# Performance work log

Measured on AMD Instinct MI355X. Metric: run time of the kernel, lower is better.

## Reference

```python
import jax, jax.numpy as jnp
import numpy as np

NUM_AGENTS = 32
N_OBS = 16
K = 5
N = 2 * NUM_AGENTS + N_OBS          # 80 nodes per graph
E_KNN = N * K                        # knn edges (loop=True)
E = E_KNN + N_OBS                    # + agent->goal edges (arange(n_obstacles) quirk of source)
AGENT_R = 0.05
OBST_SIZES = np.full((N_OBS,), 0.1, dtype=np.float32)
HID = 128


def _build_graph(obstacle_pos, agent_pos, goal_pos, agent_vel):
    # pos: agents, goals, obstacles
    pos = jnp.concatenate([agent_pos, goal_pos, obstacle_pos], axis=0)        # [N,2]
    d2 = jnp.sum((pos[:, None, :] - pos[None, :, :]) ** 2, axis=-1)           # [N,N]
    _, nbr = jax.lax.top_k(-d2, K)                                            # [N,K] k-NN incl self
    knn_src = nbr.reshape(-1)
    knn_dst = jnp.repeat(jnp.arange(N), K)
    ag_src = jnp.arange(N_OBS)
    ag_dst = ag_src + NUM_AGENTS
    src = jnp.concatenate([knn_src, ag_src])                                  # [E]
    dst = jnp.concatenate([knn_dst, ag_dst])
    # torch.unique(edge_index, dim=-1) dedup: knn edges are unique by construction;
    # only appended agent->goal edges can duplicate -> mask them out.
    dup = ((ag_src * N + ag_dst)[:, None] == (knn_src * N + knn_dst)[None, :]).any(axis=-1)
    mask = jnp.concatenate([jnp.ones((E_KNN,), dtype=bool), ~dup])
    radius = jnp.zeros((N,)).at[:NUM_AGENTS].set(AGENT_R).at[2 * NUM_AGENTS:].set(jnp.asarray(OBST_SIZES))
    x = jnp.zeros((N, 5))
    x = x.at[:NUM_AGENTS, 0].set(1.0)
    x = x.at[NUM_AGENTS:2 * NUM_AGENTS, 1].set(1.0)
    x = x.at[2 * NUM_AGENTS:, 2].set(1.0)
    x = x.at[:NUM_AGENTS, 3].set(jnp.linalg.norm(agent_vel, axis=-1))
    x = x.at[:, 4].set(radius)
    pd = pos[src] - pos[dst]
    dist = jnp.linalg.norm(pd, axis=-1)
    vel = jnp.zeros((N, 2)).at[:NUM_AGENTS].set(agent_vel)
    rv = vel[src] - vel[dst]
    pdn = pd / jnp.maximum(dist, 1e-6)[:, None]
    flag = ((src < NUM_AGENTS) & (dst == src + NUM_AGENTS)).astype(pos.dtype)
    ea = jnp.stack([flag, dist, dist - (radius[src] + radius[dst]),
                    jnp.sum(rv * pdn, axis=-1),
                    rv[:, 0] * pdn[:, 1] - rv[:, 1] * pdn[:, 0]], axis=-1)     # [E,5]
    return x, src, dst, ea, mask


def _gatv2(x, src, dst, ea, mask, Wl, bl, Wr, br, We, att, bias):
    # GATv2Conv, heads=1, add_self_loops=False, edge_dim=5
    xl = x @ Wl + bl                                    # [N,F] (messages)
    xr = x @ Wr + br                                    # [N,F]
    e = jax.nn.leaky_relu(xl[src] + xr[dst] + ea @ We, 0.2)   # [E,F]
    logit = e @ att                                     # [E]
    logit = jnp.where(mask, logit, jnp.finfo(logit.dtype).min)
    m = jax.ops.segment_max(logit, dst, num_segments=N)
    a = jnp.where(mask, jnp.exp(logit - m[dst]), 0.0)
    denom = jax.ops.segment_sum(a, dst, num_segments=N)
    alpha = a / denom[dst]
    out = jax.ops.segment_sum(alpha[:, None] * xl[src], dst, num_segments=N)
    return out + bias


def _forward_single(obstacle_pos, agent_pos, goal_pos, agent_vel, params):
    x, src, dst, ea, mask = _build_graph(obstacle_pos, agent_pos, goal_pos, agent_vel)
    h = x
    for i, p in enumerate(params):
        h = _gatv2(h, src, dst, ea, mask, *p)
        if i < len(params) - 1:
            h = jax.nn.relu(h)
    # global_add_pool over agent nodes (agents are first NUM_AGENTS nodes)
    return jnp.sum(h[:NUM_AGENTS, 0])


def reference(obstacle_pos, agent_pos, goal_pos, agent_vel,
              Wl1, bl1, Wr1, br1, We1, att1, bias1,
              Wl2, bl2, Wr2, br2, We2, att2, bias2,
              Wl3, bl3, Wr3, br3, We3, att3, bias3):
    params = [(Wl1, bl1, Wr1, br1, We1, att1, bias1),
              (Wl2, bl2, Wr2, br2, We2, att2, bias2),
              (Wl3, bl3, Wr3, br3, We3, att3, bias3)]
    vals = jax.vmap(lambda o, a, g, v: _forward_single(o, a, g, v, params))(
        obstacle_pos, agent_pos, goal_pos, agent_vel)                       # [B]
    B = vals.shape[0]
    return jnp.broadcast_to(vals[:, None, None], (B, NUM_AGENTS, 1))


def setup_inputs() -> dict:
    key = jax.random.key(0)
    ks = jax.random.split(key, 32)
    B = 1024
    inp = {
        "obstacle_pos": jax.random.normal(ks[0], (B, N_OBS, 2), dtype=jnp.float32),
        "agent_pos": jax.random.normal(ks[1], (B, NUM_AGENTS, 2), dtype=jnp.float32),
        "goal_pos": jax.random.normal(ks[2], (B, NUM_AGENTS, 2), dtype=jnp.float32),
        "agent_vel": jax.random.normal(ks[3], (B, NUM_AGENTS, 2), dtype=jnp.float32) * 0.1,
    }
    dims = [(5, HID), (HID, HID), (HID, 1)]
    ki = 4
    for li, (fi, fo) in enumerate(dims, start=1):
        s = float(np.sqrt(2.0 / (fi + fo)))
        se = float(np.sqrt(2.0 / (5 + fo)))
        inp[f"Wl{li}"] = jax.random.normal(ks[ki], (fi, fo)) * s; ki += 1
        inp[f"bl{li}"] = jnp.zeros((fo,))
        inp[f"Wr{li}"] = jax.random.normal(ks[ki], (fi, fo)) * s; ki += 1
        inp[f"br{li}"] = jnp.zeros((fo,))
        inp[f"We{li}"] = jax.random.normal(ks[ki], (5, fo)) * se; ki += 1
        inp[f"att{li}"] = jax.random.normal(ks[ki], (fo,)) * float(1.0 / np.sqrt(fo)); ki += 1
        inp[f"bias{li}"] = jnp.zeros((fo,))
    return inp
```

## Files before the change

### kernel.cpp

```cpp
#include <hip/hip_runtime.h>
#include <math.h>

typedef float floatx4 __attribute__((ext_vector_type(4)));
typedef short bf16x8  __attribute__((ext_vector_type(8)));

#define NAG   32
#define NOBS  16
#define NN    80
#define KK    5
#define EKNN  400
#define ED    416
#define HID   128
#define TPB   1024

__device__ __forceinline__ int bsw(int n, int c) { return c ^ ((n & 7) << 1); }

__device__ __forceinline__ float bfhi_f(unsigned u) {
    union { unsigned u; float f; } v; v.u = u & 0xffff0000u; return v.f;
}
__device__ __forceinline__ float bflo_f(unsigned u) {
    union { unsigned u; float f; } v; v.u = u << 16; return v.f;
}
__device__ __forceinline__ unsigned f_bf_rne(float f) {
    union { float f; unsigned u; } v; v.f = f;
    return (v.u + 0x7fffu + ((v.u >> 16) & 1u)) >> 16;
}
__device__ __forceinline__ uint2 pack_bf4v(floatx4 a) {
    uint2 r;
    r.x = f_bf_rne(a[0]) | (f_bf_rne(a[1]) << 16);
    r.y = f_bf_rne(a[2]) | (f_bf_rne(a[3]) << 16);
    return r;
}
__device__ __forceinline__ floatx4 unpack_bf4v(uint2 p) {
    floatx4 r;
    r[0] = bflo_f(p.x); r[1] = bfhi_f(p.x);
    r[2] = bflo_f(p.y); r[3] = bfhi_f(p.y);
    return r;
}

__device__ __forceinline__ void nl_pass5(const float* xf,
    const float* __restrict__ W, const float* __restrict__ bv,
    uint2* dstB, int t)
{
    const int q  = t & 31;
    const int ng = t >> 5;
    const int n0 = ng, n1 = ng + 32, n2 = 64 + (ng & 15);
    floatx4 a0 = {0.f,0.f,0.f,0.f}, a1 = a0, a2 = a0;
#pragma unroll
    for (int fi = 0; fi < 5; ++fi) {
        floatx4 wv = *(const floatx4*)(W + fi*HID + q*4);
        a0 += xf[n0*5 + fi] * wv;
        a1 += xf[n1*5 + fi] * wv;
        a2 += xf[n2*5 + fi] * wv;
    }
    floatx4 b4 = *(const floatx4*)(bv + q*4);
    a0 += b4; a1 += b4; a2 += b4;
    dstB[n0*32 + bsw(n0, q)] = pack_bf4v(a0);
    dstB[n1*32 + bsw(n1, q)] = pack_bf4v(a1);
    if (ng < 16) dstB[n2*32 + bsw(n2, q)] = pack_bf4v(a2);
}

__device__ __forceinline__ void store_tile(floatx4 ac, int mtbase, int l, int col,
                                           float bval, char* dbase)
{
#pragma unroll
    for (int rr = 0; rr < 4; rr++) {
        int row = mtbase + ((l >> 4) << 2) + rr;
        int ch  = (col >> 2) ^ ((row & 7) << 1);
        *(unsigned short*)(dbase + row*256 + ch*8 + (col & 3)*2) =
            (unsigned short)f_bf_rne(ac[rr] + bval);
    }
}

__device__ __forceinline__ void edge_logits(const uint2* xlB, const uint2* xrB,
    const float* eaS, const int* nbr, const int* gmask,
    const float* weS, const float* attS, float* logitS, int t)
{
    const int q   = t & 31;
    const int grp = t >> 5;

#pragma unroll 1
    for (int i = 0; i < 13; i++) {
        int e = grp*13 + i;
        int src, dst; bool act = true;
        if (e < EKNN) { dst = e / KK; src = nbr[e]; }
        else { int j = e - EKNN; src = j; dst = j + NAG; act = (gmask[j] != 0); }
        floatx4 sv = unpack_bf4v(xlB[src*32 + bsw(src, q)])
                   + unpack_bf4v(xrB[dst*32 + bsw(dst, q)]);
#pragma unroll
        for (int j = 0; j < 5; j++) {
            float ej = eaS[e*5 + j];
            sv += ej * ((const floatx4*)weS)[j*32 + q];
        }
        floatx4 at = ((const floatx4*)attS)[q];
        float part = 0.f;
#pragma unroll
        for (int c = 0; c < 4; c++) {
            float s = fmaxf(sv[c], 0.2f*sv[c]);
            part += s * at[c];
        }
        part += __shfl_xor(part, 16);
        part += __shfl_xor(part, 8);
        part += __shfl_xor(part, 4);
        part += __shfl_xor(part, 2);
        part += __shfl_xor(part, 1);
        if (q == 0 && act) logitS[e] = part;
    }
}

__device__ __forceinline__ void seg_softmax(const float* logitS, const int* gmask,
                                            float* alphaS, int t)
{
    if (t < NN) {
        const int n = t;
        float l[KK];
#pragma unroll
        for (int k = 0; k < KK; k++) l[k] = logitS[n*KK + k];
        float m = l[0];
#pragma unroll
        for (int k = 1; k < KK; k++) m = fmaxf(m, l[k]);
        int ge = -1; float lg = 0.f;
        if (n >= NAG && n < NAG + NOBS && gmask[n - NAG]) {
            ge = EKNN + (n - NAG);
            lg = logitS[ge];
            m = fmaxf(m, lg);
        }
        float s = 0.f, av[KK];
#pragma unroll
        for (int k = 0; k < KK; k++) { av[k] = expf(l[k] - m); s += av[k]; }
        float ag = 0.f;
        if (ge >= 0) { ag = expf(lg - m); s += ag; }
        float inv = 1.f / s;
#pragma unroll
        for (int k = 0; k < KK; k++) alphaS[n*KK + k] = av[k]*inv;
        if (ge >= 0) alphaS[ge] = ag*inv;
    }
}

__device__ __forceinline__ void aggregate(const uint2* xlB, const float* alphaS,
                                          const int* nbr, const int* gmask,
                                          const float* __restrict__ bias,
                                          uint2* hxr, int t)
{
    for (int idx = t; idx < NN*32; idx += TPB) {
        int n = idx >> 5;
        int c = idx & 31;
        floatx4 acc = *(const floatx4*)(bias + 4*c);
#pragma unroll
        for (int k = 0; k < KK; k++) {
            float a = alphaS[n*KK + k];
            int s = nbr[n*KK + k];
            acc += a * unpack_bf4v(xlB[s*32 + bsw(s, c)]);
        }
        if (n >= NAG && n < NAG + NOBS && gmask[n - NAG]) {
            float a = alphaS[EKNN + (n - NAG)];
            int s = n - NAG;
            acc += a * unpack_bf4v(xlB[s*32 + bsw(s, c)]);
        }
#pragma unroll
        for (int c2 = 0; c2 < 4; c2++) acc[c2] = fmaxf(acc[c2], 0.f);
        hxr[n*32 + bsw(n, c)] = pack_bf4v(acc);
    }
}

__global__ __launch_bounds__(TPB, 8) void e3_kernel(
    const float* __restrict__ obst, const float* __restrict__ apos,
    const float* __restrict__ gpos, const float* __restrict__ avel,
    const float* __restrict__ Wl1, const float* __restrict__ bl1,
    const float* __restrict__ Wr1, const float* __restrict__ br1,
    const float* __restrict__ We1, const float* __restrict__ att1, const float* __restrict__ bias1,
    const float* __restrict__ Wl2, const float* __restrict__ bl2,
    const float* __restrict__ Wr2, const float* __restrict__ br2,
    const float* __restrict__ We2, const float* __restrict__ att2, const float* __restrict__ bias2,
    const float* __restrict__ Wl3, const float* __restrict__ bl3,
    const float* __restrict__ Wr3, const float* __restrict__ br3,
    const float* __restrict__ We3, const float* __restrict__ att3, const float* __restrict__ bias3,
    float* __restrict__ out)
{
    __shared__ float pos0[NN], pos1[NN], vel0[NN], vel1[NN], rad[NN];
    __shared__ float xfeat[NN*5];
    __shared__ int   nbr[NN*KK];
    __shared__ int   gmask[NOBS];
    __shared__ float eaS[ED*5];
    __shared__ float logitS[ED];
    __shared__ float alphaS[ED];
    __shared__ uint2 hxrS[NN*32];
    __shared__ uint2 xlB[NN*32];
    __shared__ uint4 BfS[2*8*64];
    __shared__ float weS[5*HID];
    __shared__ float attS[HID];
    __shared__ float xl3S[NN], xr3S[NN];
    __shared__ float resS;

    const int g = blockIdx.x;
    const int t = threadIdx.x;

    if (t < NN) {
        int n = t;
        float px, py, vx = 0.f, vy = 0.f, r;
        if (n < NAG) {
            px = apos[(g*NAG + n)*2 + 0]; py = apos[(g*NAG + n)*2 + 1];
            vx = avel[(g*NAG + n)*2 + 0]; vy = avel[(g*NAG + n)*2 + 1];
            r = 0.05f;
        } else if (n < 2*NAG) {
            int m = n - NAG;
            px = gpos[(g*NAG + m)*2 + 0]; py = gpos[(g*NAG + m)*2 + 1];
            r = 0.f;
        } else {
            int m = n - 2*NAG;
            px = obst[(g*NOBS + m)*2 + 0]; py = obst[(g*NOBS + m)*2 + 1];
            r = 0.1f;
        }
        pos0[n] = px; pos1[n] = py; vel0[n] = vx; vel1[n] = vy; rad[n] = r;
        xfeat[n*5 + 0] = (n < NAG) ? 1.f : 0.f;
        xfeat[n*5 + 1] = (n >= NAG && n < 2*NAG) ? 1.f : 0.f;
        xfeat[n*5 + 2] = (n >= 2*NAG) ? 1.f : 0.f;
        xfeat[n*5 + 3] = (n < NAG) ? sqrtf(__fadd_rn(__fmul_rn(vx,vx), __fmul_rn(vy,vy))) : 0.f;
        xfeat[n*5 + 4] = r;
    }
    __syncthreads();

    if (t < NN) {
        const int i = t;
        float bd[KK]; int bi[KK];
#pragma unroll
        for (int k = 0; k < KK; k++) { bd[k] = 3.4e38f; bi[k] = -1; }
        const float pix = pos0[i], piy = pos1[i];
        for (int j = 0; j < NN; j++) {
            float dx = __fsub_rn(pix, pos0[j]);
            float dy = __fsub_rn(piy, pos1[j]);
            float d2 = __fadd_rn(__fmul_rn(dx,dx), __fmul_rn(dy,dy));
            if (d2 < bd[KK-1]) {
                int p = KK - 1;
                while (p > 0 && d2 < bd[p-1]) { bd[p] = bd[p-1]; bi[p] = bi[p-1]; p--; }
                bd[p] = d2; bi[p] = j;
            }
        }
#pragma unroll
        for (int k = 0; k < KK; k++) nbr[i*KK + k] = bi[k];
    }
    __syncthreads();

    if (t < NOBS) {
        int j = t, dup = 0;
#pragma unroll
        for (int k = 0; k < KK; k++) dup |= (nbr[(NAG + j)*KK + k] == j);
        gmask[j] = !dup;
    }
    __syncthreads();

    for (int e = t; e < ED; e += TPB) {
        int src, dst;
        if (e < EKNN) { dst = e / KK; src = nbr[e]; }
        else          { src = e - EKNN; dst = src + NAG; }
        float pdx = pos0[src] - pos0[dst];
        float pdy = pos1[src] - pos1[dst];
        float dist = sqrtf(pdx*pdx + pdy*pdy);
        float inv = 1.f / fmaxf(dist, 1e-6f);
        float pnx = pdx * inv, pny = pdy * inv;
        float rvx = vel0[src] - vel0[dst];
        float rvy = vel1[src] - vel1[dst];
        eaS[e*5 + 0] = (src < NAG && dst == src + NAG) ? 1.f : 0.f;
        eaS[e*5 + 1] = dist;
        eaS[e*5 + 2] = dist - (rad[src] + rad[dst]);
        eaS[e*5 + 3] = rvx*pnx + rvy*pny;
        eaS[e*5 + 4] = rvx*pny - rvy*pnx;
    }
    __syncthreads();

    for (int i = t; i < 5*HID; i += TPB) weS[i] = We1[i];
    for (int i = t; i < HID;  i += TPB) attS[i] = att1[i];
    nl_pass5(xfeat, Wl1, bl1, xlB,  t);
    nl_pass5(xfeat, Wr1, br1, hxrS, t);
    __syncthreads();
    edge_logits(xlB, hxrS, eaS, nbr, gmask, weS, attS, logitS, t);
    __syncthreads();
    seg_softmax(logitS, gmask, alphaS, t);
    __syncthreads();
    aggregate(xlB, alphaS, nbr, gmask, bias1, hxrS, t);
    __syncthreads();

    for (int i = t; i < 5*HID; i += TPB) weS[i] = We2[i];
    for (int i = t; i < HID;  i += TPB) attS[i] = att2[i];
    {
        const int w   = t >> 6;
        const int l   = t & 63;
        const int mat = w >> 3;
        const int nt  = w & 7;
        const int ar  = l & 15;
        const int kg2 = (l >> 4) << 1;
        const int arx = (ar & 7) << 1;

        const int sm = t >> 9;
        const int s  = t & 511;
        const int sn = s & 127;
        const int g8 = s >> 7;
        const float* __restrict__ Wst = sm ? Wr2 : Wl2;
        const int swidx = sm*512 + (sn >> 4)*64 + ((sn & 15) | (g8 << 4));

        floatx4 acc0 = {0.f,0.f,0.f,0.f}, acc1 = acc0, acc2 = acc0,
                acc3 = acc0, acc4 = acc0;

#pragma unroll 1
        for (int kb = 0; kb < 4; ++kb) {
            const float* wp = Wst + (kb*32 + g8*8)*HID + sn;
            uint4 pk;
            pk.x = f_bf_rne(wp[0])     | (f_bf_rne(wp[HID])   << 16);
            pk.y = f_bf_rne(wp[2*HID]) | (f_bf_rne(wp[3*HID]) << 16);
            pk.z = f_bf_rne(wp[4*HID]) | (f_bf_rne(wp[5*HID]) << 16);
            pk.w = f_bf_rne(wp[6*HID]) | (f_bf_rne(wp[7*HID]) << 16);
            BfS[swidx] = pk;
            __syncthreads();

            bf16x8 bfrag = ((const bf16x8*)BfS)[mat*512 + nt*64 + l];
            const char* hbase = (const char*)hxrS;
            const int cA = ((kb*8 + kg2) ^ arx) * 8;
#define MT_MFMA(AC, MT) { \
            bf16x8 af = *(const bf16x8*)(hbase + (MT*4096) + ar*256 + cA); \
            AC = __builtin_amdgcn_mfma_f32_16x16x32_bf16(af, bfrag, AC, 0, 0, 0); }
            MT_MFMA(acc0, 0)
            MT_MFMA(acc1, 1)
            MT_MFMA(acc2, 2)
            MT_MFMA(acc3, 3)
            MT_MFMA(acc4, 4)
#undef MT_MFMA
            __syncthreads();
        }

        const float* __restrict__ bv = mat ? br2 : bl2;
        char* dbase = (char*)(mat ? hxrS : xlB);
        const int col = nt*16 + ar;
        const float bval = bv[col];
        store_tile(acc0,  0, l, col, bval, dbase);
        store_tile(acc1, 16, l, col, bval, dbase);
        store_tile(acc2, 32, l, col, bval, dbase);
        store_tile(acc3, 48, l, col, bval, dbase);
        store_tile(acc4, 64, l, col, bval, dbase);
    }
    __syncthreads();

    edge_logits(xlB, hxrS, eaS, nbr, gmask, weS, attS, logitS, t);
    __syncthreads();
    seg_softmax(logitS, gmask, alphaS, t);
    __syncthreads();
    aggregate(xlB, alphaS, nbr, gmask, bias2, hxrS, t);
    __syncthreads();

    {
        const int q   = t & 31;
        const int grp = t >> 5;
        floatx4 wl4 = *(const floatx4*)(Wl3 + q*4);
        floatx4 wr4 = *(const floatx4*)(Wr3 + q*4);
#pragma unroll
        for (int rep = 0; rep < 3; rep++) {
            int n = grp + rep*32;
            if (n < NN) {
                floatx4 hv = unpack_bf4v(hxrS[n*32 + bsw(n, q)]);
                float al = hv[0]*wl4[0] + hv[1]*wl4[1] + hv[2]*wl4[2] + hv[3]*wl4[3];
                float ar3 = hv[0]*wr4[0] + hv[1]*wr4[1] + hv[2]*wr4[2] + hv[3]*wr4[3];
                al += __shfl_xor(al, 16); ar3 += __shfl_xor(ar3, 16);
                al += __shfl_xor(al, 8);  ar3 += __shfl_xor(ar3, 8);
                al += __shfl_xor(al, 4);  ar3 += __shfl_xor(ar3, 4);
                al += __shfl_xor(al, 2);  ar3 += __shfl_xor(ar3, 2);
                al += __shfl_xor(al, 1);  ar3 += __shfl_xor(ar3, 1);
                if (q == 0) {
                    xl3S[n] = al + bl3[0];
                    xr3S[n] = ar3 + br3[0];
                }
            }
        }
    }
    __syncthreads();

    {
        float w0 = We3[0], w1 = We3[1], w2 = We3[2], w3 = We3[3], w4 = We3[4];
        float a0 = att3[0];
        for (int e = t; e < ED; e += TPB) {
            int src, dst;
            if (e < EKNN) { dst = e / KK; src = nbr[e]; }
            else { src = e - EKNN; dst = src + NAG; if (!gmask[src]) continue; }
            float s = xl3S[src] + xr3S[dst]
                    + eaS[e*5+0]*w0 + eaS[e*5+1]*w1 + eaS[e*5+2]*w2
                    + eaS[e*5+3]*w3 + eaS[e*5+4]*w4;
            s = fmaxf(s, 0.2f*s);
            logitS[e] = s * a0;
        }
    }
    __syncthreads();

    seg_softmax(logitS, gmask, alphaS, t);
    __syncthreads();

    float v = 0.f;
    if (t < NAG) {
        v = bias3[0];
#pragma unroll
        for (int k = 0; k < KK; k++) v += alphaS[t*KK + k] * xl3S[nbr[t*KK + k]];
    }
    if (t < 64) {
#pragma unroll
        for (int o = 32; o > 0; o >>= 1) v += __shfl_xor(v, o);
        if (t == 0) resS = v;
    }
    __syncthreads();
    if (t < NAG) out[g*NAG + t] = resS;
}

extern "C" void kernel_launch(void* const* d_in, const int* in_sizes, int n_in,
                              void* d_out, int out_size, void* d_ws, size_t ws_size,
                              hipStream_t stream)
{
    const float* obst = (const float*)d_in[0];
    const float* apos = (const float*)d_in[1];
    const float* gpos = (const float*)d_in[2];
    const float* avel = (const float*)d_in[3];
    const int B = in_sizes[1] / (NAG * 2);

    e3_kernel<<<B, TPB, 0, stream>>>(
        obst, apos, gpos, avel,
        (const float*)d_in[4],  (const float*)d_in[5],  (const float*)d_in[6],
        (const float*)d_in[7],  (const float*)d_in[8],  (const float*)d_in[9],
        (const float*)d_in[10],
        (const float*)d_in[11], (const float*)d_in[12], (const float*)d_in[13],
        (const float*)d_in[14], (const float*)d_in[15], (const float*)d_in[16],
        (const float*)d_in[17],
        (const float*)d_in[18], (const float*)d_in[19], (const float*)d_in[20],
        (const float*)d_in[21], (const float*)d_in[22], (const float*)d_in[23],
        (const float*)d_in[24],
        (float*)d_out);
}
```

Baseline: 129.3 us.

## Compute GATv2 edge logits with bf16 MFMA for edge-attribute projection

Replaces the scalar per-edge edge_logits loop with an MFMA-based version. The edge attributes times We are computed by 16x16x32 bf16 MFMA tiles instead of per-lane FMAs, and src/dst indices are packed into a shared array. Edge attributes and We are converted to bf16 and stored in the reused BfS buffer. This is meant to cut ALU and shared-memory traffic in the logit stage, at the cost of bf16 rounding of edge features and weights, more packing work, and a fixed 16-edge tile mapping.

Result: faster. 116.6 us (median of 2 runs) (-9.9%).

```diff
diff --git a/kernel.cpp b/kernel.cpp
--- a/kernel.cpp
+++ b/kernel.cpp
@@ -72,39 +72,47 @@
     }
 }
 
-__device__ __forceinline__ void edge_logits(const uint2* xlB, const uint2* xrB,
-    const float* eaS, const int* nbr, const int* gmask,
-    const float* weS, const float* attS, float* logitS, int t)
-{
-    const int q   = t & 31;
-    const int grp = t >> 5;
+__device__ __forceinline__ void edge_mfma(const uint2* xlB, const uint2* xrB,
+    const uint4* WeBfT, const uint4* eaB, const unsigned short* sdS,
+    const int* gmask, const float* attS, float* logitS, int t)
+{
+    const int w = t >> 6, l = t & 63;
+    const int g = l >> 4, e16 = l & 15;
+    const bf16x8 zf = {0,0,0,0,0,0,0,0};
 
 #pragma unroll 1
-    for (int i = 0; i < 13; i++) {
-        int e = grp*13 + i;
-        int src, dst; bool act = true;
-        if (e < EKNN) { dst = e / KK; src = nbr[e]; }
-        else { int j = e - EKNN; src = j; dst = j + NAG; act = (gmask[j] != 0); }
-        floatx4 sv = unpack_bf4v(xlB[src*32 + bsw(src, q)])
-                   + unpack_bf4v(xrB[dst*32 + bsw(dst, q)]);
-#pragma unroll
-        for (int j = 0; j < 5; j++) {
-            float ej = eaS[e*5 + j];
-            sv += ej * ((const floatx4*)weS)[j*32 + q];
-        }
-        floatx4 at = ((const floatx4*)attS)[q];
-        float part = 0.f;
-#pragma unroll
-        for (int c = 0; c < 4; c++) {
-            float s = fmaxf(sv[c], 0.2f*sv[c]);
-            part += s * at[c];
-        }
-        part += __shfl_xor(part, 16);
-        part += __shfl_xor(part, 8);
-        part += __shfl_xor(part, 4);
-        part += __shfl_xor(part, 2);
-        part += __shfl_xor(part, 1);
-        if (q == 0 && act) logitS[e] = part;
+    for (int rep = 0; rep < 2; rep++) {
+        const int mt = w + rep*16;
+        if (mt >= 26) break;
+        const int e = mt*16 + e16;
+        const unsigned sdv = sdS[e];
+        const int src = sdv & 0xff, dst = sdv >> 8;
+        const int sb = src*32, db = dst*32;
+        const int sx = (src & 7) << 1, dx = (dst & 7) << 1;
+        bf16x8 bfrag = (l < 16) ? ((const bf16x8*)eaB)[e] : zf;
+        float partial = 0.f;
+
+#pragma unroll 1
+        for (int ct = 0; ct < 8; ct++) {
+            bf16x8 afrag = (l < 16) ? ((const bf16x8*)WeBfT)[ct*16 + e16] : zf;
+            floatx4 D = {0.f,0.f,0.f,0.f};
+            D = __builtin_amdgcn_mfma_f32_16x16x32_bf16(afrag, bfrag, D, 0, 0, 0);
+            floatx4 attv = ((const floatx4*)attS)[ct*4 + g];
+            floatx4 xlv = unpack_bf4v(xlB[sb + ((4*ct + g) ^ sx)]);
+            floatx4 xrv = unpack_bf4v(xrB[db + ((4*ct + g) ^ dx)]);
+#pragma unroll
+            for (int rr = 0; rr < 4; rr++) {
+                float s = D[rr] + xlv[rr] + xrv[rr];
+                float m = fmaxf(s, 0.2f*s);
+                partial = fmaf(m, attv[rr], partial);
+            }
+        }
+        partial += __shfl_xor(partial, 16);
+        partial += __shfl_xor(partial, 32);
+        if (l < 16) {
+            bool act = (e < EKNN) || (gmask[e - EKNN] != 0);
+            if (act) logitS[e] = partial;
+        }
     }
 }
 
@@ -184,13 +192,16 @@
     __shared__ float eaS[ED*5];
     __shared__ float logitS[ED];
     __shared__ float alphaS[ED];
+    __shared__ unsigned short sdS[ED];
     __shared__ uint2 hxrS[NN*32];
     __shared__ uint2 xlB[NN*32];
     __shared__ uint4 BfS[2*8*64];
-    __shared__ float weS[5*HID];
     __shared__ float attS[HID];
     __shared__ float xl3S[NN], xr3S[NN];
     __shared__ float resS;
+
+    uint4* WeBfT = BfS;
+    uint4* eaB   = BfS + 128;
 
     const int g = blockIdx.x;
     const int t = threadIdx.x;
@@ -260,28 +271,44 @@
         float pnx = pdx * inv, pny = pdy * inv;
         float rvx = vel0[src] - vel0[dst];
         float rvy = vel1[src] - vel1[dst];
-        eaS[e*5 + 0] = (src < NAG && dst == src + NAG) ? 1.f : 0.f;
-        eaS[e*5 + 1] = dist;
-        eaS[e*5 + 2] = dist - (rad[src] + rad[dst]);
-        eaS[e*5 + 3] = rvx*pnx + rvy*pny;
-        eaS[e*5 + 4] = rvx*pny - rvy*pnx;
-    }
-    __syncthreads();
-
-    for (int i = t; i < 5*HID; i += TPB) weS[i] = We1[i];
-    for (int i = t; i < HID;  i += TPB) attS[i] = att1[i];
+        float e0 = (src < NAG && dst == src + NAG) ? 1.f : 0.f;
+        float e1 = dist;
+        float e2 = dist - (rad[src] + rad[dst]);
+        float e3 = rvx*pnx + rvy*pny;
+        float e4 = rvx*pny - rvy*pnx;
+        eaS[e*5 + 0] = e0; eaS[e*5 + 1] = e1; eaS[e*5 + 2] = e2;
+        eaS[e*5 + 3] = e3; eaS[e*5 + 4] = e4;
+        sdS[e] = (unsigned short)(src | (dst << 8));
+        uint4 pk;
+        pk.x = f_bf_rne(e0) | (f_bf_rne(e1) << 16);
+        pk.y = f_bf_rne(e2) | (f_bf_rne(e3) << 16);
+        pk.z = f_bf_rne(e4);
+        pk.w = 0u;
+        eaB[e] = pk;
+    }
+
+    if (t < HID) {
+        uint4 pw;
+        pw.x = f_bf_rne(We1[0*HID + t]) | (f_bf_rne(We1[1*HID + t]) << 16);
+        pw.y = f_bf_rne(We1[2*HID + t]) | (f_bf_rne(We1[3*HID + t]) << 16);
+        pw.z = f_bf_rne(We1[4*HID + t]);
+        pw.w = 0u;
+        WeBfT[t] = pw;
+        attS[t] = att1[t];
+    }
+    __syncthreads();
+
     nl_pass5(xfeat, Wl1, bl1, xlB,  t);
     nl_pass5(xfeat, Wr1, br1, hxrS, t);
     __syncthreads();
-    edge_logits(xlB, hxrS, eaS, nbr, gmask, weS, attS, logitS, t);
+    edge_mfma(xlB, hxrS, WeBfT, eaB, sdS, gmask, attS, logitS, t);
     __syncthreads();
     seg_softmax(logitS, gmask, alphaS, t);
     __syncthreads();
     aggregate(xlB, alphaS, nbr, gmask, bias1, hxrS, t);
     __syncthreads();
 
-    for (int i = t; i < 5*HID; i += TPB) weS[i] = We2[i];
-    for (int i = t; i < HID;  i += TPB) attS[i] = att2[i];
+    if (t < HID) attS[t] = att2[t];
     {
         const int w   = t >> 6;
         const int l   = t & 63;
@@ -337,9 +364,26 @@
         store_tile(acc3, 48, l, col, bval, dbase);
         store_tile(acc4, 64, l, col, bval, dbase);
     }
-    __syncthreads();
-
-    edge_logits(xlB, hxrS, eaS, nbr, gmask, weS, attS, logitS, t);
+
+    if (t < HID) {
+        uint4 pw;
+        pw.x = f_bf_rne(We2[0*HID + t]) | (f_bf_rne(We2[1*HID + t]) << 16);
+        pw.y = f_bf_rne(We2[2*HID + t]) | (f_bf_rne(We2[3*HID + t]) << 16);
+        pw.z = f_bf_rne(We2[4*HID + t]);
+        pw.w = 0u;
+        WeBfT[t] = pw;
+    } else if (t < HID + ED) {
+        int e = t - HID;
+        uint4 pk;
+        pk.x = f_bf_rne(eaS[e*5+0]) | (f_bf_rne(eaS[e*5+1]) << 16);
+        pk.y = f_bf_rne(eaS[e*5+2]) | (f_bf_rne(eaS[e*5+3]) << 16);
+        pk.z = f_bf_rne(eaS[e*5+4]);
+        pk.w = 0u;
+        eaB[e] = pk;
+    }
+    __syncthreads();
+
+    edge_mfma(xlB, hxrS, WeBfT, eaB, sdS, gmask, attS, logitS, t);
     __syncthreads();
     seg_softmax(logitS, gmask, alphaS, t);
     __syncthreads();
```
